# Kernel tuning notes

Hardware: AMD Instinct MI355X
Metric: run time of the kernel (lower is better)

The kernel has to match this reference:

```python
import jax, jax.numpy as jnp
import numpy as np

N, M, P, BATCH, T = 32, 8, 16, 64, 128
STD_DYN = 0.1
STD_OBS = 0.1


def _mT(x):
    return jnp.swapaxes(x, -1, -2)


def _sym(x):
    return 0.5 * (x + _mT(x))


def setup_inputs() -> dict:
    key = jax.random.key(0)
    ks = jax.random.split(key, 5)
    Y = jax.random.normal(ks[0], (BATCH, T, P), jnp.float32)
    U = jax.random.normal(ks[1], (BATCH, T, M), jnp.float32)
    # scale A so spectral radius < 1 -> stable covariance recursion over T steps
    A = jax.random.normal(ks[2], (BATCH, T, N, N), jnp.float32) * (0.5 / np.sqrt(N))
    B_mat = jax.random.normal(ks[3], (BATCH, T, N, M), jnp.float32) * 0.1
    C = jax.random.normal(ks[4], (BATCH, T, P, N), jnp.float32) * (1.0 / np.sqrt(N))
    mu0 = jnp.zeros((N,), jnp.float32)
    Sigma0 = jnp.eye(N, dtype=jnp.float32)  # SPD initial covariance
    return {"Y": Y, "U": U, "A": A, "B_mat": B_mat, "C": C, "mu0": mu0, "Sigma0": Sigma0}


def _kalman_smooth(Y, U, A, B_mat, C, mu0, Sigma0):
    b, t = Y.shape[0], Y.shape[1]
    n = mu0.shape[0]
    p = Y.shape[-1]
    dt = Y.dtype
    Q = (STD_DYN ** 2) * jnp.eye(n, dtype=dt)
    R = (STD_OBS ** 2) * jnp.eye(p, dtype=dt)
    I = jnp.eye(n, dtype=dt)
    tm = lambda x: jnp.moveaxis(x, 0, 1)  # [B,T,...] -> [T,B,...]

    # ---- forward filter (lax.scan over time, batched over B) ----
    def fstep(carry, x):
        mu, Sig = carry  # [b,n], [b,n,n]
        y, u, At, Bt, Ct = x
        mu_p = jnp.einsum('bij,bj->bi', At, mu) + jnp.einsum('bij,bj->bi', Bt, u)
        Sig_p = At @ Sig @ _mT(At) + Q
        r = y - jnp.einsum('bij,bj->bi', Ct, mu_p)
        S = _sym(Ct @ Sig_p @ _mT(Ct) + R)  # [b,p,p]
        # K = Sig_p C^T S^{-1}  (matches torch: solve(S, PCT.mT).mT)
        K = _mT(jnp.linalg.solve(S, _mT(Sig_p @ _mT(Ct))))  # [b,n,p]
        mu_f = mu_p + jnp.einsum('bij,bj->bi', K, r)
        IKC = I - K @ Ct
        Sig_f = _sym(IKC @ Sig_p @ _mT(IKC) + K @ R @ _mT(K))
        return (mu_f, Sig_f), (mu_f, Sig_f, mu_p, Sig_p)

    init = (jnp.broadcast_to(mu0, (b, n)), jnp.broadcast_to(Sigma0, (b, n, n)))
    A_tm = tm(A)
    _, (mu_f, Sig_f, mu_p, Sig_p) = jax.lax.scan(
        fstep, init, (tm(Y), tm(U), A_tm, tm(B_mat), tm(C)))

    # ---- RTS smoother (reverse scan) ----
    def sstep(carry, x):
        mu_s, Sig_s = carry
        Sf, Sp1, mf, mp1, At = x
        # J = Sig_f A^T Sig_pred^{-1} (matches torch: solve(Sp1.mT, (Sf@A.mT).mT).mT)
        J = _mT(jnp.linalg.solve(_mT(Sp1), _mT(Sf @ _mT(At))))
        mu_n = mf + jnp.einsum('bij,bj->bi', J, mu_s - mp1)
        Sig_n = _sym(Sf + J @ (Sig_s - Sp1) @ _mT(J))
        return (mu_n, Sig_n), (mu_n, Sig_n)

    xs = (Sig_f[:-1], Sig_p[1:], mu_f[:-1], mu_p[1:], A_tm[:-1])
    _, (mu_sm, Sig_sm) = jax.lax.scan(
        sstep, (mu_f[-1], Sig_f[-1]), xs, reverse=True)
    mu_sm = jnp.concatenate([mu_sm, mu_f[-1:]], axis=0)   # [T,b,n]
    Sig_sm = jnp.concatenate([Sig_sm, Sig_f[-1:]], axis=0)  # [T,b,n,n]
    mu_sm = jnp.moveaxis(mu_sm, 0, 1)
    Sig_sm = jnp.moveaxis(Sig_sm, 0, 1)
    # pack smoothed means + covariances into one array: [B,T,n,1+n]
    return jnp.concatenate([mu_sm[..., None], Sig_sm], axis=-1)


def reference(Y, U, A, B_mat, C, mu0, Sigma0):
    return _kalman_smooth(Y, U, A, B_mat, C, mu0, Sigma0)
```

## Files before the change

### kernel.cpp

```cpp
#include <hip/hip_runtime.h>

#define TT 128
#define NB 64
#define NSZ 32
#define MSZ 8
#define PSZ 16

typedef __attribute__((ext_vector_type(8)))  short bf16x8;
typedef __attribute__((ext_vector_type(16))) float f32x16;
typedef __attribute__((ext_vector_type(4)))  float f32x4;
typedef __attribute__((ext_vector_type(4)))  unsigned int uint4v;
typedef __attribute__((ext_vector_type(2)))  unsigned int uint2v;

union U8 { uint4v u; bf16x8 b; };

__device__ __forceinline__ float frcp(float x){ return __builtin_amdgcn_rcpf(x); }
__device__ __forceinline__ float rdl(float x, int lane){
  return __int_as_float(__builtin_amdgcn_readlane(__float_as_int(x), lane));
}

__device__ __forceinline__ unsigned int hipack(float x0, float x1){
  return __builtin_amdgcn_perm(__float_as_uint(x1), __float_as_uint(x0), 0x07060302u);
}
__device__ __forceinline__ unsigned int lopack(float x0, float x1){
  float l0 = x0 - __uint_as_float(__float_as_uint(x0) & 0xFFFF0000u);
  float l1 = x1 - __uint_as_float(__float_as_uint(x1) & 0xFFFF0000u);
  return __builtin_amdgcn_perm(__float_as_uint(l1), __float_as_uint(l0), 0x07060302u);
}
__device__ __forceinline__ unsigned int packhl(float x){
  unsigned int u = __float_as_uint(x);
  unsigned int h = u & 0xFFFF0000u;
  float xl = x - __uint_as_float(h);
  return h | (__float_as_uint(xl) >> 16);
}
__device__ __forceinline__ float unpk(unsigned int u){
  return __uint_as_float(u & 0xFFFF0000u) + __uint_as_float(u << 16);
}
__device__ __forceinline__ uint4v frag_hi(uint4v a, uint4v b){
  uint4v r;
  r.x = __builtin_amdgcn_perm(a.y, a.x, 0x07060302u);
  r.y = __builtin_amdgcn_perm(a.w, a.z, 0x07060302u);
  r.z = __builtin_amdgcn_perm(b.y, b.x, 0x07060302u);
  r.w = __builtin_amdgcn_perm(b.w, b.z, 0x07060302u);
  return r;
}
__device__ __forceinline__ uint4v frag_lo(uint4v a, uint4v b){
  uint4v r;
  r.x = __builtin_amdgcn_perm(a.y, a.x, 0x05040100u);
  r.y = __builtin_amdgcn_perm(a.w, a.z, 0x05040100u);
  r.z = __builtin_amdgcn_perm(b.y, b.x, 0x05040100u);
  r.w = __builtin_amdgcn_perm(b.w, b.z, 0x05040100u);
  return r;
}
__device__ __forceinline__ float blof(unsigned int h, unsigned int l){
  return __uint_as_float(h << 16) + __uint_as_float(l << 16);
}
__device__ __forceinline__ float bhif(unsigned int h, unsigned int l){
  return __uint_as_float(h & 0xFFFF0000u) + __uint_as_float(l & 0xFFFF0000u);
}
__device__ __forceinline__ f32x16 mfma32(bf16x8 a, bf16x8 b, f32x16 c){
  return __builtin_amdgcn_mfma_f32_32x32x16_bf16(a, b, c, 0, 0, 0);
}
__device__ __forceinline__ f32x4 mfma16(bf16x8 a, bf16x8 b, f32x4 c){
  return __builtin_amdgcn_mfma_f32_16x16x32_bf16(a, b, c, 0, 0, 0);
}
__device__ __forceinline__ void split16(float4 v0, float4 v1, float4 v2, float4 v3,
                                        unsigned short* hi, unsigned short* lo){
  uint4v hw0, hw1, lw0, lw1;
  hw0.x=hipack(v0.x,v0.y); hw0.y=hipack(v0.z,v0.w); hw0.z=hipack(v1.x,v1.y); hw0.w=hipack(v1.z,v1.w);
  hw1.x=hipack(v2.x,v2.y); hw1.y=hipack(v2.z,v2.w); hw1.z=hipack(v3.x,v3.y); hw1.w=hipack(v3.z,v3.w);
  lw0.x=lopack(v0.x,v0.y); lw0.y=lopack(v0.z,v0.w); lw0.z=lopack(v1.x,v1.y); lw0.w=lopack(v1.z,v1.w);
  lw1.x=lopack(v2.x,v2.y); lw1.y=lopack(v2.z,v2.w); lw1.z=lopack(v3.x,v3.y); lw1.w=lopack(v3.z,v3.w);
  *(uint4v*)hi = hw0; *(uint4v*)(hi+8) = hw1;
  *(uint4v*)lo = lw0; *(uint4v*)(lo+8) = lw1;
}
__device__ __forceinline__ void split8(float4 v0, float4 v1,
                                       unsigned short* hi, unsigned short* lo){
  uint4v hw, lw;
  hw.x=hipack(v0.x,v0.y); hw.y=hipack(v0.z,v0.w); hw.z=hipack(v1.x,v1.y); hw.w=hipack(v1.z,v1.w);
  lw.x=lopack(v0.x,v0.y); lw.y=lopack(v0.z,v0.w); lw.z=lopack(v1.x,v1.y); lw.w=lopack(v1.z,v1.w);
  *(uint4v*)hi = hw; *(uint4v*)lo = lw;
}
#define MK8(v0, v1, HI, LO) do { \
  (HI).u.x = hipack((v0).x,(v0).y); (HI).u.y = hipack((v0).z,(v0).w); \
  (HI).u.z = hipack((v1).x,(v1).y); (HI).u.w = hipack((v1).z,(v1).w); \
  (LO).u.x = lopack((v0).x,(v0).y); (LO).u.y = lopack((v0).z,(v0).w); \
  (LO).u.z = lopack((v1).x,(v1).y); (LO).u.w = lopack((v1).z,(v1).w); \
} while(0)

#define DLAYOUT_TO_BFRAG(uu, h, B_H0, B_L0, B_H1, B_L1) do { \
  float sw_[16]; \
  _Pragma("unroll") \
  for (int r_=0;r_<16;++r_) sw_[r_] = __shfl_xor((uu)[r_], 32); \
  float v0_[8], v1_[8]; \
  v0_[0]=(h)? sw_[4] :(uu)[0];  v0_[1]=(h)? sw_[5] :(uu)[1]; \
  v0_[2]=(h)? sw_[6] :(uu)[2];  v0_[3]=(h)? sw_[7] :(uu)[3]; \
  v0_[4]=(h)? (uu)[4]:sw_[0];   v0_[5]=(h)? (uu)[5]:sw_[1]; \
  v0_[6]=(h)? (uu)[6]:sw_[2];   v0_[7]=(h)? (uu)[7]:sw_[3]; \
  v1_[0]=(h)? sw_[12]:(uu)[8];  v1_[1]=(h)? sw_[13]:(uu)[9]; \
  v1_[2]=(h)? sw_[14]:(uu)[10]; v1_[3]=(h)? sw_[15]:(uu)[11]; \
  v1_[4]=(h)? (uu)[12]:sw_[8];  v1_[5]=(h)? (uu)[13]:sw_[9]; \
  v1_[6]=(h)? (uu)[14]:sw_[10]; v1_[7]=(h)? (uu)[15]:sw_[11]; \
  (B_H0).u.x=hipack(v0_[0],v0_[1]); (B_H0).u.y=hipack(v0_[2],v0_[3]); \
  (B_H0).u.z=hipack(v0_[4],v0_[5]); (B_H0).u.w=hipack(v0_[6],v0_[7]); \
  (B_L0).u.x=lopack(v0_[0],v0_[1]); (B_L0).u.y=lopack(v0_[2],v0_[3]); \
  (B_L0).u.z=lopack(v0_[4],v0_[5]); (B_L0).u.w=lopack(v0_[6],v0_[7]); \
  (B_H1).u.x=hipack(v1_[0],v1_[1]); (B_H1).u.y=hipack(v1_[2],v1_[3]); \
  (B_H1).u.z=hipack(v1_[4],v1_[5]); (B_H1).u.w=hipack(v1_[6],v1_[7]); \
  (B_L1).u.x=lopack(v1_[0],v1_[1]); (B_L1).u.y=lopack(v1_[2],v1_[3]); \
  (B_L1).u.z=lopack(v1_[4],v1_[5]); (B_L1).u.w=lopack(v1_[6],v1_[7]); \
} while(0)

__global__ __launch_bounds__(64) void kf_forward(
    const float* __restrict__ Yg, const float* __restrict__ Ug,
    const float* __restrict__ Ag, const float* __restrict__ Bg,
    const float* __restrict__ Cg, const float* __restrict__ mu0g,
    const float* __restrict__ Sig0g,
    float* __restrict__ outg, float* __restrict__ wsSig, float* __restrict__ wsMu)
{
  const int l   = threadIdx.x;
  const int b   = blockIdx.x;
  const int c32 = l & 31;
  const int h   = l >> 5;
  const int c16 = l & 15;
  const int q4  = l >> 4;
  const int kofA = h * 8;
  const int kofC = q4 * 8;
  const int rA = l >> 1, cA = (l & 1) << 4;
  const int rC = l >> 2, cC = (l & 3) << 3;

  __shared__ __align__(16) unsigned short Ahi[32][40], Alo[32][40];
  __shared__ __align__(16) unsigned short Chi[16][40], Clo[16][40];
  __shared__ __align__(16) unsigned short Ghi[32][40], Glo[32][40];
  __shared__ __align__(16) unsigned short Phi[32][40], Plo[32][40];
  __shared__ __align__(16) unsigned short Yhi[32][24], Ylo[32][24];
  __shared__ __align__(16) unsigned int   ZP[16][40];
  __shared__ __align__(16) unsigned int   KtTP[32][26];
  __shared__ __align__(16) float SLf[16][20];
  __shared__ __align__(16) float CSf[16][40];
  __shared__ __align__(16) float Bm[32][12];
  __shared__ __align__(16) float muf[32], mupf[32], rvf[16], yvf[16], uvf[8];

  const size_t bt0 = (size_t)b * TT;

  {
    const float* ap = Ag + bt0*1024 + rA*32 + cA;
    split16(*(const float4*)(ap+0), *(const float4*)(ap+4),
            *(const float4*)(ap+8), *(const float4*)(ap+12),
            &Ahi[rA][cA], &Alo[rA][cA]);
    const float* sp0 = Sig0g + rA*32 + cA;
    split16(*(const float4*)(sp0+0), *(const float4*)(sp0+4),
            *(const float4*)(sp0+8), *(const float4*)(sp0+12),
            &Ghi[rA][cA], &Glo[rA][cA]);
    const float* cp = Cg + bt0*512 + rC*32 + cC;
    split8(*(const float4*)(cp+0), *(const float4*)(cp+4),
           &Chi[rC][cC], &Clo[rC][cC]);
    *(float4*)&Bm[l>>1][(l&1)*4] = *(const float4*)(Bg + bt0*256 + (l>>1)*8 + (l&1)*4);
    if (l < 32) muf[l] = mu0g[l];
    if (l < 16) yvf[l] = Yg[bt0*16 + l];
    if (l < 8)  uvf[l] = Ug[bt0*8 + l];
  }

  for (int t = 0; t < TT; ++t) {
    const size_t bt = bt0 + t;

    U8 a_h0, a_h1, a_l0, a_l1, s_h0, s_h1, s_l0, s_l1;
    a_h0.u = *(const uint4v*)&Ahi[c32][0  + kofA];
    a_h1.u = *(const uint4v*)&Ahi[c32][16 + kofA];
    a_l0.u = *(const uint4v*)&Alo[c32][0  + kofA];
    a_l1.u = *(const uint4v*)&Alo[c32][16 + kofA];
    s_h0.u = *(const uint4v*)&Ghi[c32][0  + kofA];
    s_h1.u = *(const uint4v*)&Ghi[c32][16 + kofA];
    s_l0.u = *(const uint4v*)&Glo[c32][0  + kofA];
    s_l1.u = *(const uint4v*)&Glo[c32][16 + kofA];
    f32x16 t1a, t1b;
    #pragma unroll
    for (int r=0;r<16;++r){ t1a[r] = 0.f; t1b[r] = 0.f; }
    t1a = mfma32(s_h0.b, a_h0.b, t1a);
    t1a = mfma32(s_h0.b, a_l0.b, t1a);
    t1a = mfma32(s_l0.b, a_h0.b, t1a);
    t1b = mfma32(s_h1.b, a_h1.b, t1b);
    t1b = mfma32(s_h1.b, a_l1.b, t1b);
    t1b = mfma32(s_l1.b, a_h1.b, t1b);
    float uu[16];
    #pragma unroll
    for (int r=0;r<16;++r) uu[r] = t1a[r] + t1b[r];
    float part = 0.f;
    {
      float4 m0 = *(const float4*)&muf[kofA];
      float4 m1 = *(const float4*)&muf[kofA+4];
      float4 m2 = *(const float4*)&muf[16+kofA];
      float4 m3 = *(const float4*)&muf[16+kofA+4];
      part = fmaf(blof(a_h0.u.x,a_l0.u.x), m0.x, part);
      part = fmaf(bhif(a_h0.u.x,a_l0.u.x), m0.y, part);
      part = fmaf(blof(a_h0.u.y,a_l0.u.y), m0.z, part);
      part = fmaf(bhif(a_h0.u.y,a_l0.u.y), m0.w, part);
      part = fmaf(blof(a_h0.u.z,a_l0.u.z), m1.x, part);
      part = fmaf(bhif(a_h0.u.z,a_l0.u.z), m1.y, part);
      part = fmaf(blof(a_h0.u.w,a_l0.u.w), m1.z, part);
      part = fmaf(bhif(a_h0.u.w,a_l0.u.w), m1.w, part);
      part = fmaf(blof(a_h1.u.x,a_l1.u.x), m2.x, part);
      part = fmaf(bhif(a_h1.u.x,a_l1.u.x), m2.y, part);
      part = fmaf(blof(a_h1.u.y,a_l1.u.y), m2.z, part);
      part = fmaf(bhif(a_h1.u.y,a_l1.u.y), m2.w, part);
      part = fmaf(blof(a_h1.u.z,a_l1.u.z), m3.x, part);
      part = fmaf(bhif(a_h1.u.z,a_l1.u.z), m3.y, part);
      part = fmaf(blof(a_h1.u.w,a_l1.u.w), m3.z, part);
      part = fmaf(bhif(a_h1.u.w,a_l1.u.w), m3.w, part);
    }
    part += __shfl_xor(part, 32);
    {
      float4 b0 = *(const float4*)&Bm[c32][0];
      float4 b1 = *(const float4*)&Bm[c32][4];
      float4 u0 = *(const float4*)&uvf[0];
      float4 u1 = *(const float4*)&uvf[4];
      part = fmaf(b0.x,u0.x, fmaf(b0.y,u0.y, fmaf(b0.z,u0.z, fmaf(b0.w,u0.w, part))));
      part = fmaf(b1.x,u1.x, fmaf(b1.y,u1.y, fmaf(b1.z,u1.z, fmaf(b1.w,u1.w, part))));
    }
    if (l < 32){ mupf[c32] = part; wsMu[bt*32 + c32] = part; }

    U8 b_h0, b_h1, b_l0, b_l1;
    DLAYOUT_TO_BFRAG(uu, h, b_h0, b_l0, b_h1, b_l1);
    f32x16 spa, spb;
    #pragma unroll
    for (int r=0;r<16;++r){ spa[r] = 0.f; spb[r] = 0.f; }
    spa = mfma32(a_h0.b, b_h0.b, spa);
    spa = mfma32(a_h0.b, b_l0.b, spa);
    spa = mfma32(a_l0.b, b_h0.b, spa);
    spb = mfma32(a_h1.b, b_h1.b, spb);
    spb = mfma32(a_h1.b, b_l1.b, spb);
    spb = mfma32(a_l1.b, b_h1.b, spb);
    f32x16 sp;
    #pragma unroll
    for (int r=0;r<16;++r){
      int rr = (r&3) + 8*(r>>2) + 4*h;
      sp[r] = spa[r] + spb[r] + ((rr == c32) ? 0.01f : 0.f);
    }
    {
      float* wp = wsSig + (bt*32 + c32)*32;
      *(float4*)(wp + 0  + 4*h) = make_float4(sp[0], sp[1], sp[2], sp[3]);
      *(float4*)(wp + 8  + 4*h) = make_float4(sp[4], sp[5], sp[6], sp[7]);
      *(float4*)(wp + 16 + 4*h) = make_float4(sp[8], sp[9], sp[10],sp[11]);
      *(float4*)(wp + 24 + 4*h) = make_float4(sp[12],sp[13],sp[14],sp[15]);
      #pragma unroll
      for (int gq=0; gq<4; ++gq){
        uint2v hw, lw;
        hw.x = hipack(sp[4*gq+0], sp[4*gq+1]); hw.y = hipack(sp[4*gq+2], sp[4*gq+3]);
        lw.x = lopack(sp[4*gq+0], sp[4*gq+1]); lw.y = lopack(sp[4*gq+2], sp[4*gq+3]);
        *(uint2v*)&Phi[c32][8*gq + 4*h] = hw;
        *(uint2v*)&Plo[c32][8*gq + 4*h] = lw;
      }
    }

    U8 c_h, c_l, p_h0, p_l0, p_h1, p_l1;
    c_h.u  = *(const uint4v*)&Chi[c16][kofC];
    c_l.u  = *(const uint4v*)&Clo[c16][kofC];
    p_h0.u = *(const uint4v*)&Phi[c16][kofC];
    p_l0.u = *(const uint4v*)&Plo[c16][kofC];
    p_h1.u = *(const uint4v*)&Phi[16+c16][kofC];
    p_l1.u = *(const uint4v*)&Plo[16+c16][kofC];
    f32x4 cs0, cs1;
    #pragma unroll
    for (int r=0;r<4;++r){ cs0[r]=0.f; cs1[r]=0.f; }
    cs0 = mfma16(c_h.b, p_h0.b, cs0);
    cs0 = mfma16(c_h.b, p_l0.b, cs0);
    cs0 = mfma16(c_l.b, p_h0.b, cs0);
    cs1 = mfma16(c_h.b, p_h1.b, cs1);
    cs1 = mfma16(c_h.b, p_l1.b, cs1);
    cs1 = mfma16(c_l.b, p_h1.b, cs1);
    #pragma unroll
    for (int r=0;r<4;++r){
      int rr = q4*4 + r;
      ZP[rr][c16]     = packhl(cs0[r]);
      ZP[rr][16+c16]  = packhl(cs1[r]);
      CSf[rr][c16]    = cs0[r];
      CSf[rr][16+c16] = cs1[r];
    }
    {
      uint2v hw0, lw0, hw1, lw1;
      hw0.x = hipack(cs0[0],cs0[1]); hw0.y = hipack(cs0[2],cs0[3]);
      lw0.x = lopack(cs0[0],cs0[1]); lw0.y = lopack(cs0[2],cs0[3]);
      hw1.x = hipack(cs1[0],cs1[1]); hw1.y = hipack(cs1[2],cs1[3]);
      lw1.x = lopack(cs1[0],cs1[1]); lw1.y = lopack(cs1[2],cs1[3]);
      *(uint2v*)&Yhi[c16][q4*4]    = hw0; *(uint2v*)&Ylo[c16][q4*4]    = lw0;
      *(uint2v*)&Yhi[16+c16][q4*4] = hw1; *(uint2v*)&Ylo[16+c16][q4*4] = lw1;
    }
    {
      float prr = 0.f;
      float4 m0 = *(const float4*)&mupf[kofC];
      float4 m1 = *(const float4*)&mupf[kofC+4];
      prr = fmaf(blof(c_h.u.x,c_l.u.x), m0.x, prr);
      prr = fmaf(bhif(c_h.u.x,c_l.u.x), m0.y, prr);
      prr = fmaf(blof(c_h.u.y,c_l.u.y), m0.z, prr);
      prr = fmaf(bhif(c_h.u.y,c_l.u.y), m0.w, prr);
      prr = fmaf(blof(c_h.u.z,c_l.u.z), m1.x, prr);
      prr = fmaf(bhif(c_h.u.z,c_l.u.z), m1.y, prr);
      prr = fmaf(blof(c_h.u.w,c_l.u.w), m1.z, prr);
      prr = fmaf(bhif(c_h.u.w,c_l.u.w), m1.w, prr);
      prr += __shfl_xor(prr, 16);
      prr += __shfl_xor(prr, 32);
      if (l < 16) rvf[l] = yvf[l] - prr;
    }

    {
      U8 z_h, z_l;
      uint4v pz0 = *(const uint4v*)&ZP[c16][kofC];
      uint4v pz1 = *(const uint4v*)&ZP[c16][kofC+4];
      z_h.u = frag_hi(pz0, pz1); z_l.u = frag_lo(pz0, pz1);
      f32x4 ss;
      #pragma unroll
      for (int r=0;r<4;++r) ss[r] = 0.f;
      ss = mfma16(z_h.b, c_h.b, ss);
      ss = mfma16(z_h.b, c_l.b, ss);
      ss = mfma16(z_l.b, c_h.b, ss);
      #pragma unroll
      for (int r=0;r<4;++r){
        int rr = q4*4 + r;
        SLf[rr][c16] = ss[r] + ((rr == c16) ? 0.01f : 0.f);
      }
    }

    float4 pa0, pa1, pa2, pa3, pc0, pc1, pbv;
    float py = 0.f, pu = 0.f;
    pa0=pa1=pa2=pa3=make_float4(0.f,0.f,0.f,0.f);
    pc0=pc1=pbv=make_float4(0.f,0.f,0.f,0.f);
    if (t + 1 < TT){
      const float* ap = Ag + (bt+1)*1024 + rA*32 + cA;
      pa0 = *(const float4*)(ap+0);  pa1 = *(const float4*)(ap+4);
      pa2 = *(const float4*)(ap+8);  pa3 = *(const float4*)(ap+12);
      const float* cp = Cg + (bt+1)*512 + rC*32 + cC;
      pc0 = *(const float4*)(cp+0);  pc1 = *(const float4*)(cp+4);
      pbv = *(const float4*)(Bg + (bt+1)*256 + (l>>1)*8 + (l&1)*4);
      if (l < 16) py = Yg[(bt+1)*16 + l];
      if (l < 8)  pu = Ug[(bt+1)*8 + l];
    }

    {
      float aug[16];
      if (l < 16){
        #pragma unroll
        for (int i=0;i<16;++i) aug[i] = 0.5f*(SLf[i][l] + SLf[l][i]);
      } else if (l < 48){
        #pragma unroll
        for (int i=0;i<16;++i) aug[i] = CSf[i][l-16];
      } else {
        #pragma unroll
        for (int i=0;i<16;++i) aug[i] = 0.f;
      }
      #pragma unroll
      for (int k=0;k<16;++k){
        float piv = rdl(aug[k], k);
        float q = -aug[k] * frcp(piv);
        #pragma unroll
        for (int i=0;i<16;++i){
          if (i == k) continue;
          float s = rdl(aug[i], k);
          aug[i] = fmaf(q, s, aug[i]);
        }
      }
      if (l >= 16 && l < 48){
        #pragma unroll
        for (int i=0;i<16;++i){
          float d = rdl(aug[i], i);
          KtTP[l-16][i] = packhl(-aug[i] * frcp(d));
        }
      }
    }

    f32x16 sf = sp;
    {
      U8 y_h, y_l, kt_h, kt_l;
      y_h.u = *(const uint4v*)&Yhi[c32][8*h];
      y_l.u = *(const uint4v*)&Ylo[c32][8*h];
      uint4v k0, k1;
      { uint2v a0 = *(const uint2v*)&KtTP[c32][8*h];
        uint2v a1 = *(const uint2v*)&KtTP[c32][8*h+2];
        uint2v a2 = *(const uint2v*)&KtTP[c32][8*h+4];
        uint2v a3 = *(const uint2v*)&KtTP[c32][8*h+6];
        k0.x=a0.x; k0.y=a0.y; k0.z=a1.x; k0.w=a1.y;
        k1.x=a2.x; k1.y=a2.y; k1.z=a3.x; k1.w=a3.y; }
      kt_h.u = frag_hi(k0, k1); kt_l.u = frag_lo(k0, k1);
      sf = mfma32(y_h.b, kt_h.b, sf);
      sf = mfma32(y_h.b, kt_l.b, sf);
      sf = mfma32(y_l.b, kt_h.b, sf);
    }
    #pragma unroll
    for (int gq=0; gq<4; ++gq){
      uint2v hw, lw;
      hw.x = hipack(sf[4*gq+0], sf[4*gq+1]); hw.y = hipack(sf[4*gq+2], sf[4*gq+3]);
      lw.x = lopack(sf[4*gq+0], sf[4*gq+1]); lw.y = lopack(sf[4*gq+2], sf[4*gq+3]);
      *(uint2v*)&Ghi[c32][8*gq + 4*h] = hw;
      *(uint2v*)&Glo[c32][8*gq + 4*h] = lw;
    }
    {
      float* ob = outg + (bt*32)*33;
      #pragma unroll
      for (int r=0;r<16;++r){
        int rr = (r&3) + 8*(r>>2) + 4*h;
        ob[rr*33 + 1 + c32] = sf[r];
      }
      float mf = mupf[c32];
      #pragma unroll
      for (int p=0;p<16;++p){
        unsigned int w = KtTP[c32][p];
        mf = fmaf(-unpk(w), rvf[p], mf);
      }
      if (l < 32){ muf[c32] = mf; ob[c32*33] = mf; }
    }

    if (t + 1 < TT){
      split16(pa0, pa1, pa2, pa3, &Ahi[rA][cA], &Alo[rA][cA]);
      split8(pc0, pc1, &Chi[rC][cC], &Clo[rC][cC]);
      *(float4*)&Bm[l>>1][(l&1)*4] = pbv;
      if (l < 16) yvf[l] = py;
      if (l < 8)  uvf[l] = pu;
    }
  }
}

__global__ __launch_bounds__(64) void kf_precomp(
    const float* __restrict__ Ag, float* __restrict__ outg,
    float* __restrict__ wsSig, const float* __restrict__ wsMu)
{
  const int t = blockIdx.x;
  const int b = blockIdx.y;
  const int l = threadIdx.x;
  const int c32 = l & 31;
  const int h = l >> 5;
  const int kofA = h * 8;

  __shared__ __align__(16) float        Sffr[1060];
  __shared__ __align__(16) unsigned int MmP[32][34];
  __shared__ __align__(16) unsigned int VPT[32][34];
  __shared__ __align__(16) unsigned int JP [32][34];
  __shared__ float mp1f[32];

  const size_t bt = (size_t)b*TT + t;
  float* osl = outg + bt*1056;

  {
    const float4* src = (const float4*)osl;
    #pragma unroll
    for (int q=0;q<4;++q) *(float4*)&Sffr[(l + 64*q)*4] = src[l + 64*q];
    if (l < 8) *(float4*)&Sffr[(l + 256)*4] = src[l + 256];
    if (l < 32) mp1f[l] = wsMu[(bt+1)*32 + l];
  }

  float aug[32];
  if (l < 32){
    const float* pp = wsSig + (bt+1)*1024 + (size_t)l*32;
    #pragma unroll
    for (int q=0;q<8;++q){
      float4 v = *(const float4*)(pp + 4*q);
      aug[4*q]=v.x; aug[4*q+1]=v.y; aug[4*q+2]=v.z; aug[4*q+3]=v.w;
    }
  } else {
    #pragma unroll
    for (int i=0;i<32;++i) aug[i] = (i == l-32) ? 1.f : 0.f;
  }

  U8 a_h0, a_l0, a_h1, a_l1;
  {
    const float* ap = Ag + bt*1024 + c32*32;
    float4 v0 = *(const float4*)(ap + kofA);
    float4 v1 = *(const float4*)(ap + kofA + 4);
    float4 v2 = *(const float4*)(ap + 16 + kofA);
    float4 v3 = *(const float4*)(ap + 16 + kofA + 4);
    MK8(v0, v1, a_h0, a_l0);
    MK8(v2, v3, a_h1, a_l1);
  }
  U8 s_h0, s_l0, s_h1, s_l1;
  {
    const float* rp = &Sffr[c32*33 + 1];
    float4 v0, v1, v2, v3;
    v0.x=rp[kofA+0]; v0.y=rp[kofA+1]; v0.z=rp[kofA+2]; v0.w=rp[kofA+3];
    v1.x=rp[kofA+4]; v1.y=rp[kofA+5]; v1.z=rp[kofA+6]; v1.w=rp[kofA+7];
    v2.x=rp[16+kofA+0]; v2.y=rp[16+kofA+1]; v2.z=rp[16+kofA+2]; v2.w=rp[16+kofA+3];
    v3.x=rp[16+kofA+4]; v3.y=rp[16+kofA+5]; v3.z=rp[16+kofA+6]; v3.w=rp[16+kofA+7];
    MK8(v0, v1, s_h0, s_l0);
    MK8(v2, v3, s_h1, s_l1);
  }

  f32x16 ma, mb;
  #pragma unroll
  for (int r=0;r<16;++r){ ma[r]=0.f; mb[r]=0.f; }
  ma = mfma32(s_h0.b, a_h0.b, ma);
  ma = mfma32(s_h0.b, a_l0.b, ma);
  ma = mfma32(s_l0.b, a_h0.b, ma);
  mb = mfma32(s_h1.b, a_h1.b, mb);
  mb = mfma32(s_h1.b, a_l1.b, mb);
  mb = mfma32(s_l1.b, a_h1.b, mb);
  #pragma unroll
  for (int r=0;r<16;++r){
    int rr = (r&3) + 8*(r>>2) + 4*h;
    MmP[rr][c32] = packhl(ma[r] + mb[r]);
  }

  #pragma unroll
  for (int k=0;k<32;++k){
    float piv = rdl(aug[k], k);
    float q = -aug[k] * frcp(piv);
    #pragma unroll
    for (int i=0;i<32;++i){
      if (i == k) continue;
      float s = rdl(aug[i], k);
      aug[i] = fmaf(q, s, aug[i]);
    }
  }
  if (l >= 32){
    #pragma unroll
    for (int i=0;i<32;++i){
      float d = rdl(aug[i], i);
      VPT[l-32][i] = packhl(aug[i] * frcp(d));
    }
  }

  U8 m_h0, m_l0, m_h1, m_l1;
  {
    uint4v ua, ub, uc, ud;
    ua.x=MmP[c32][kofA+0]; ua.y=MmP[c32][kofA+1]; ua.z=MmP[c32][kofA+2]; ua.w=MmP[c32][kofA+3];
    ub.x=MmP[c32][kofA+4]; ub.y=MmP[c32][kofA+5]; ub.z=MmP[c32][kofA+6]; ub.w=MmP[c32][kofA+7];
    uc.x=MmP[c32][16+kofA+0]; uc.y=MmP[c32][16+kofA+1]; uc.z=MmP[c32][16+kofA+2]; uc.w=MmP[c32][16+kofA+3];
    ud.x=MmP[c32][16+kofA+4]; ud.y=MmP[c32][16+kofA+5]; ud.z=MmP[c32][16+kofA+6]; ud.w=MmP[c32][16+kofA+7];
    m_h0.u = frag_hi(ua, ub); m_l0.u = frag_lo(ua, ub);
    m_h1.u = frag_hi(uc, ud); m_l1.u = frag_lo(uc, ud);
  }
  U8 v_h0, v_l0, v_h1, v_l1;
  {
    uint4v ua, ub, uc, ud;
    ua.x=VPT[c32][kofA+0]; ua.y=VPT[c32][kofA+1]; ua.z=VPT[c32][kofA+2]; ua.w=VPT[c32][kofA+3];
    ub.x=VPT[c32][kofA+4]; ub.y=VPT[c32][kofA+5]; ub.z=VPT[c32][kofA+6]; ub.w=VPT[c32][kofA+7];
    uc.x=VPT[c32][16+kofA+0]; uc.y=VPT[c32][16+kofA+1]; uc.z=VPT[c32][16+kofA+2]; uc.w=VPT[c32][16+kofA+3];
    ud.x=VPT[c32][16+kofA+4]; ud.y=VPT[c32][16+kofA+5]; ud.z=VPT[c32][16+kofA+6]; ud.w=VPT[c32][16+kofA+7];
    v_h0.u = frag_hi(ua, ub); v_l0.u = frag_lo(ua, ub);
    v_h1.u = frag_hi(uc, ud); v_l1.u = frag_lo(uc, ud);
  }
  f32x16 ja, jb;
  #pragma unroll
  for (int r=0;r<16;++r){ ja[r]=0.f; jb[r]=0.f; }
  ja = mfma32(m_h0.b, v_h0.b, ja);
  ja = mfma32(m_h0.b, v_l0.b, ja);
  ja = mfma32(m_l0.b, v_h0.b, ja);
  jb = mfma32(m_h1.b, v_h1.b, jb);
  jb = mfma32(m_h1.b, v_l1.b, jb);
  jb = mfma32(m_l1.b, v_h1.b, jb);
  {
    float* jws = wsSig + (bt+1)*1024;
    #pragma unroll
    for (int r=0;r<16;++r){
      int rr = (r&3) + 8*(r>>2) + 4*h;
      float jv = ja[r] + jb[r];
      jws[rr*32 + c32] = jv;
      JP[rr][c32] = packhl(-jv);
    }
  }

  U8 nj_h0, nj_l0, nj_h1, nj_l1;
  {
    uint4v ua, ub, uc, ud;
    ua.x=JP[c32][kofA+0]; ua.y=JP[c32][kofA+1]; ua.z=JP[c32][kofA+2]; ua.w=JP[c32][kofA+3];
    ub.x=JP[c32][kofA+4]; ub.y=JP[c32][kofA+5]; ub.z=JP[c32][kofA+6]; ub.w=JP[c32][kofA+7];
    uc.x=JP[c32][16+kofA+0]; uc.y=JP[c32][16+kofA+1]; uc.z=JP[c32][16+kofA+2]; uc.w=JP[c32][16+kofA+3];
    ud.x=JP[c32][16+kofA+4]; ud.y=JP[c32][16+kofA+5]; ud.z=JP[c32][16+kofA+6]; ud.w=JP[c32][16+kofA+7];
    nj_h0.u = frag_hi(ua, ub); nj_l0.u = frag_lo(ua, ub);
    nj_h1.u = frag_hi(uc, ud); nj_l1.u = frag_lo(uc, ud);
  }
  f32x16 ea, eb;
  #pragma unroll
  for (int r=0;r<16;++r){
    int rr = (r&3) + 8*(r>>2) + 4*h;
    ea[r] = Sffr[rr*33 + 1 + c32];
    eb[r] = 0.f;
  }
  ea = mfma32(m_h0.b, nj_h0.b, ea);
  ea = mfma32(m_h0.b, nj_l0.b, ea);
  ea = mfma32(m_l0.b, nj_h0.b, ea);
  eb = mfma32(m_h1.b, nj_h1.b, eb);
  eb = mfma32(m_h1.b, nj_l1.b, eb);
  eb = mfma32(m_l1.b, nj_h1.b, eb);
  #pragma unroll
  for (int r=0;r<16;++r){
    int rr = (r&3) + 8*(r>>2) + 4*h;
    osl[rr*33 + 1 + c32] = ea[r] + eb[r];
  }

  {
    float e2 = Sffr[c32*33];
    #pragma unroll
    for (int k=0;k<32;++k)
      e2 = fmaf(unpk(JP[c32][k]), mp1f[k], e2);
    if (l < 32) osl[c32*33] = e2;
  }
}

__global__ __launch_bounds__(64) void kf_backward(
    float* __restrict__ outg, const float* __restrict__ wsSig)
{
  const int l   = threadIdx.x;
  const int b   = blockIdx.x;
  const int c32 = l & 31;
  const int h   = l >> 5;
  const int kofA = h * 8;
  const int rA = l >> 1, cA = (l & 1) << 4;

  __shared__ __align__(16) unsigned short Jhi[32][40], Jlo[32][40];
  __shared__ __align__(16) unsigned int   SP[32][36];
  __shared__ float muv[32];

  const size_t base = (size_t)b * TT;

  float er[16]; float ev;
  {
    const float* os = outg + (base + TT - 1)*32*33;
    const float* rp = os + rA*33 + 1 + cA;
    float4 v0 = *(const float4*)(rp+0), v1 = *(const float4*)(rp+4),
           v2 = *(const float4*)(rp+8), v3 = *(const float4*)(rp+12);
    uint4v u0, u1;
    u0.x = packhl(v0.x); u0.y = packhl(v0.y); u0.z = packhl(v0.z); u0.w = packhl(v0.w);
    u1.x = packhl(v1.x); u1.y = packhl(v1.y); u1.z = packhl(v1.z); u1.w = packhl(v1.w);
    *(uint4v*)&SP[rA][cA+0] = u0; *(uint4v*)&SP[rA][cA+4] = u1;
    u0.x = packhl(v2.x); u0.y = packhl(v2.y); u0.z = packhl(v2.z); u0.w = packhl(v2.w);
    u1.x = packhl(v3.x); u1.y = packhl(v3.y); u1.z = packhl(v3.z); u1.w = packhl(v3.w);
    *(uint4v*)&SP[rA][cA+8] = u0; *(uint4v*)&SP[rA][cA+12] = u1;
    if (l < 32) muv[l] = os[l*33];
    const float* jp = wsSig + ((base + TT - 1)*32 + rA)*32 + cA;
    split16(*(const float4*)(jp+0), *(const float4*)(jp+4),
            *(const float4*)(jp+8), *(const float4*)(jp+12),
            &Jhi[rA][cA], &Jlo[rA][cA]);
    const float* oe = outg + (base + TT - 2)*32*33;
    #pragma unroll
    for (int r=0;r<16;++r){
      int rr = (r&3) + 8*(r>>2) + 4*h;
      er[r] = oe[rr*33 + 1 + c32];
    }
    ev = (l < 32) ? oe[l*33] : 0.f;
  }

  for (int t = TT - 2; t >= 0; --t) {
    float4 pj0, pj1, pj2, pj3; float ner[16]; float nev = 0.f;
    if (t > 0) {
      const float* jp = wsSig + ((base + t)*32 + rA)*32 + cA;
      pj0 = *(const float4*)(jp+0);  pj1 = *(const float4*)(jp+4);
      pj2 = *(const float4*)(jp+8);  pj3 = *(const float4*)(jp+12);
      const float* oe = outg + (base + t - 1)*32*33;
      #pragma unroll
      for (int r=0;r<16;++r){
        int rr = (r&3) + 8*(r>>2) + 4*h;
        ner[r] = oe[rr*33 + 1 + c32];
      }
      if (l < 32) nev = oe[l*33];
    } else {
      pj0=pj1=pj2=pj3=make_float4(0.f,0.f,0.f,0.f);
      #pragma unroll
      for (int r=0;r<16;++r) ner[r] = 0.f;
    }

    U8 a_h0, a_h1, a_l0, a_l1;
    a_h0.u = *(const uint4v*)&Jhi[c32][0  + kofA];
    a_h1.u = *(const uint4v*)&Jhi[c32][16 + kofA];
    a_l0.u = *(const uint4v*)&Jlo[c32][0  + kofA];
    a_l1.u = *(const uint4v*)&Jlo[c32][16 + kofA];
    U8 s_h0, s_l0, s_h1, s_l1;
    {
      uint4v ua = *(const uint4v*)&SP[c32][0  + kofA];
      uint4v ub = *(const uint4v*)&SP[c32][4  + kofA];
      uint4v uc = *(const uint4v*)&SP[c32][16 + kofA];
      uint4v ud = *(const uint4v*)&SP[c32][20 + kofA];
      s_h0.u = frag_hi(ua, ub); s_l0.u = frag_lo(ua, ub);
      s_h1.u = frag_hi(uc, ud); s_l1.u = frag_lo(uc, ud);
    }
    f32x16 wa, wb;
    #pragma unroll
    for (int r=0;r<16;++r){ wa[r]=0.f; wb[r]=0.f; }
    wa = mfma32(s_h0.b, a_h0.b, wa);
    wa = mfma32(s_h0.b, a_l0.b, wa);
    wa = mfma32(s_l0.b, a_h0.b, wa);
    wb = mfma32(s_h1.b, a_h1.b, wb);
    wb = mfma32(s_h1.b, a_l1.b, wb);
    wb = mfma32(s_l1.b, a_h1.b, wb);
    float ww[16];
    #pragma unroll
    for (int r=0;r<16;++r) ww[r] = wa[r] + wb[r];

    U8 bw_h0, bw_l0, bw_h1, bw_l1;
    DLAYOUT_TO_BFRAG(ww, h, bw_h0, bw_l0, bw_h1, bw_l1);
    f32x16 ga, gb;
    #pragma unroll
    for (int r=0;r<16;++r){ ga[r] = er[r]; gb[r] = 0.f; }
    ga = mfma32(a_h0.b, bw_h0.b, ga);
    ga = mfma32(a_h0.b, bw_l0.b, ga);
    ga = mfma32(a_l0.b, bw_h0.b, ga);
    gb = mfma32(a_h1.b, bw_h1.b, gb);
    gb = mfma32(a_h1.b, bw_l1.b, gb);
    gb = mfma32(a_l1.b, bw_h1.b, gb);

    float part = 0.f;
    {
      float4 m0 = *(const float4*)&muv[kofA];
      float4 m1 = *(const float4*)&muv[kofA+4];
      float4 m2 = *(const float4*)&muv[16+kofA];
      float4 m3 = *(const float4*)&muv[16+kofA+4];
      part = fmaf(blof(a_h0.u.x,a_l0.u.x), m0.x, part);
      part = fmaf(bhif(a_h0.u.x,a_l0.u.x), m0.y, part);
      part = fmaf(blof(a_h0.u.y,a_l0.u.y), m0.z, part);
      part = fmaf(bhif(a_h0.u.y,a_l0.u.y), m0.w, part);
      part = fmaf(blof(a_h0.u.z,a_l0.u.z), m1.x, part);
      part = fmaf(bhif(a_h0.u.z,a_l0.u.z), m1.y, part);
      part = fmaf(blof(a_h0.u.w,a_l0.u.w), m1.z, part);
      part = fmaf(bhif(a_h0.u.w,a_l0.u.w), m1.w, part);
      part = fmaf(blof(a_h1.u.x,a_l1.u.x), m2.x, part);
      part = fmaf(bhif(a_h1.u.x,a_l1.u.x), m2.y, part);
      part = fmaf(blof(a_h1.u.y,a_l1.u.y), m2.z, part);
      part = fmaf(bhif(a_h1.u.y,a_l1.u.y), m2.w, part);
      part = fmaf(blof(a_h1.u.z,a_l1.u.z), m3.x, part);
      part = fmaf(bhif(a_h1.u.z,a_l1.u.z), m3.y, part);
      part = fmaf(blof(a_h1.u.w,a_l1.u.w), m3.z, part);
      part = fmaf(bhif(a_h1.u.w,a_l1.u.w), m3.w, part);
    }
    part += __shfl_xor(part, 32);
    float mn = ev + part;

    {
      float* ob = outg + ((base + t)*32)*33;
      #pragma unroll
      for (int r=0;r<16;++r){
        int rr = (r&3) + 8*(r>>2) + 4*h;
        ob[rr*33 + 1 + c32] = ga[r] + gb[r];
      }
      #pragma unroll
      for (int gq=0; gq<4; ++gq){
        uint4v uw;
        uw.x = packhl(ga[4*gq+0]+gb[4*gq+0]); uw.y = packhl(ga[4*gq+1]+gb[4*gq+1]);
        uw.z = packhl(ga[4*gq+2]+gb[4*gq+2]); uw.w = packhl(ga[4*gq+3]+gb[4*gq+3]);
        *(uint4v*)&SP[c32][8*gq + 4*h] = uw;
      }
      if (l < 32){ muv[l] = mn; ob[l*33] = mn; }
    }

    if (t > 0){
      split16(pj0, pj1, pj2, pj3, &Jhi[rA][cA], &Jlo[rA][cA]);
      #pragma unroll
      for (int r=0;r<16;++r) er[r] = ner[r];
      ev = nev;
    }
  }
}

extern "C" void kernel_launch(void* const* d_in, const int* in_sizes, int n_in,
                              void* d_out, int out_size, void* d_ws, size_t ws_size,
                              hipStream_t stream) {
  (void)in_sizes; (void)n_in; (void)out_size; (void)ws_size;
  const float* Yg   = (const float*)d_in[0];
  const float* Ug   = (const float*)d_in[1];
  const float* Ag   = (const float*)d_in[2];
  const float* Bg   = (const float*)d_in[3];
  const float* Cg   = (const float*)d_in[4];
  const float* mu0g = (const float*)d_in[5];
  const float* S0g  = (const float*)d_in[6];
  float* outg = (float*)d_out;
  float* wsSig = (float*)d_ws;
  float* wsMu  = wsSig + (size_t)NB*TT*NSZ*NSZ;

  hipLaunchKernelGGL(kf_forward, dim3(NB), dim3(64), 0, stream,
                     Yg, Ug, Ag, Bg, Cg, mu0g, S0g, outg, wsSig, wsMu);
  hipLaunchKernelGGL(kf_precomp, dim3(TT-1, NB), dim3(64), 0, stream,
                     Ag, outg, wsSig, wsMu);
  hipLaunchKernelGGL(kf_backward, dim3(NB), dim3(64), 0, stream,
                     outg, wsSig);
}
```

Baseline: 704.0 us.

## Process two batches per wavefront in backward smoother and load J directly to registers

The backward RTS kernel now has each 64-thread block run two independent batch recursions interleaved, so the launch uses half as many blocks. Interleaving the two chains is meant to hide MFMA and memory latency along the serial time dependence. J fragments are loaded straight from global memory into registers and split into bf16 hi/lo parts in registers, which removes the Jhi/Jlo shared-memory staging. The cost is more register pressure and only 32 workgroups, which occupy fewer CUs. MK8 is assumed to be defined in the part of the file not shown.

```diff
diff --git a/kernel.cpp b/kernel.cpp
--- a/kernel.cpp
+++ b/kernel.cpp
@@ -597,151 +597,171 @@
     float* __restrict__ outg, const float* __restrict__ wsSig)
 {
   const int l   = threadIdx.x;
-  const int b   = blockIdx.x;
   const int c32 = l & 31;
   const int h   = l >> 5;
   const int kofA = h * 8;
   const int rA = l >> 1, cA = (l & 1) << 4;
 
-  __shared__ __align__(16) unsigned short Jhi[32][40], Jlo[32][40];
-  __shared__ __align__(16) unsigned int   SP[32][36];
-  __shared__ float muv[32];
-
-  const size_t base = (size_t)b * TT;
-
-  float er[16]; float ev;
-  {
-    const float* os = outg + (base + TT - 1)*32*33;
+  __shared__ __align__(16) unsigned int SP[2][32][36];
+  __shared__ float muv[2][32];
+
+  size_t base[2];
+  base[0] = (size_t)(blockIdx.x*2 + 0) * TT;
+  base[1] = (size_t)(blockIdx.x*2 + 1) * TT;
+
+  float er[2][16]; float ev[2];
+  float4 pj[2][4];
+
+  #pragma unroll
+  for (int bb=0;bb<2;++bb){
+    const float* os = outg + (base[bb] + TT - 1)*1056;
     const float* rp = os + rA*33 + 1 + cA;
     float4 v0 = *(const float4*)(rp+0), v1 = *(const float4*)(rp+4),
            v2 = *(const float4*)(rp+8), v3 = *(const float4*)(rp+12);
     uint4v u0, u1;
     u0.x = packhl(v0.x); u0.y = packhl(v0.y); u0.z = packhl(v0.z); u0.w = packhl(v0.w);
     u1.x = packhl(v1.x); u1.y = packhl(v1.y); u1.z = packhl(v1.z); u1.w = packhl(v1.w);
-    *(uint4v*)&SP[rA][cA+0] = u0; *(uint4v*)&SP[rA][cA+4] = u1;
+    *(uint4v*)&SP[bb][rA][cA+0] = u0; *(uint4v*)&SP[bb][rA][cA+4] = u1;
     u0.x = packhl(v2.x); u0.y = packhl(v2.y); u0.z = packhl(v2.z); u0.w = packhl(v2.w);
     u1.x = packhl(v3.x); u1.y = packhl(v3.y); u1.z = packhl(v3.z); u1.w = packhl(v3.w);
-    *(uint4v*)&SP[rA][cA+8] = u0; *(uint4v*)&SP[rA][cA+12] = u1;
-    if (l < 32) muv[l] = os[l*33];
-    const float* jp = wsSig + ((base + TT - 1)*32 + rA)*32 + cA;
-    split16(*(const float4*)(jp+0), *(const float4*)(jp+4),
-            *(const float4*)(jp+8), *(const float4*)(jp+12),
-            &Jhi[rA][cA], &Jlo[rA][cA]);
-    const float* oe = outg + (base + TT - 2)*32*33;
+    *(uint4v*)&SP[bb][rA][cA+8] = u0; *(uint4v*)&SP[bb][rA][cA+12] = u1;
+    if (l < 32) muv[bb][l] = os[l*33];
+    const float* jp = wsSig + (base[bb] + TT - 1)*1024 + c32*32;
+    pj[bb][0] = *(const float4*)(jp + kofA);
+    pj[bb][1] = *(const float4*)(jp + kofA + 4);
+    pj[bb][2] = *(const float4*)(jp + 16 + kofA);
+    pj[bb][3] = *(const float4*)(jp + 16 + kofA + 4);
+    const float* oe = outg + (base[bb] + TT - 2)*1056;
     #pragma unroll
     for (int r=0;r<16;++r){
       int rr = (r&3) + 8*(r>>2) + 4*h;
-      er[r] = oe[rr*33 + 1 + c32];
-    }
-    ev = (l < 32) ? oe[l*33] : 0.f;
+      er[bb][r] = oe[rr*33 + 1 + c32];
+    }
+    ev[bb] = (l < 32) ? oe[l*33] : 0.f;
   }
 
   for (int t = TT - 2; t >= 0; --t) {
-    float4 pj0, pj1, pj2, pj3; float ner[16]; float nev = 0.f;
+    float4 nj[2][4]; float ner[2][16]; float nev[2];
     if (t > 0) {
-      const float* jp = wsSig + ((base + t)*32 + rA)*32 + cA;
-      pj0 = *(const float4*)(jp+0);  pj1 = *(const float4*)(jp+4);
-      pj2 = *(const float4*)(jp+8);  pj3 = *(const float4*)(jp+12);
-      const float* oe = outg + (base + t - 1)*32*33;
-      #pragma unroll
-      for (int r=0;r<16;++r){
-        int rr = (r&3) + 8*(r>>2) + 4*h;
-        ner[r] = oe[rr*33 + 1 + c32];
-      }
-      if (l < 32) nev = oe[l*33];
+      #pragma unroll
+      for (int bb=0;bb<2;++bb){
+        const float* jp = wsSig + (base[bb] + t)*1024 + c32*32;
+        nj[bb][0] = *(const float4*)(jp + kofA);
+        nj[bb][1] = *(const float4*)(jp + kofA + 4);
+        nj[bb][2] = *(const float4*)(jp + 16 + kofA);
+        nj[bb][3] = *(const float4*)(jp + 16 + kofA + 4);
+        const float* oe = outg + (base[bb] + t - 1)*1056;
+        #pragma unroll
+        for (int r=0;r<16;++r){
+          int rr = (r&3) + 8*(r>>2) + 4*h;
+          ner[bb][r] = oe[rr*33 + 1 + c32];
+        }
+        nev[bb] = (l < 32) ? oe[l*33] : 0.f;
+      }
     } else {
-      pj0=pj1=pj2=pj3=make_float4(0.f,0.f,0.f,0.f);
-      #pragma unroll
-      for (int r=0;r<16;++r) ner[r] = 0.f;
-    }
-
-    U8 a_h0, a_h1, a_l0, a_l1;
-    a_h0.u = *(const uint4v*)&Jhi[c32][0  + kofA];
-    a_h1.u = *(const uint4v*)&Jhi[c32][16 + kofA];
-    a_l0.u = *(const uint4v*)&Jlo[c32][0  + kofA];
-    a_l1.u = *(const uint4v*)&Jlo[c32][16 + kofA];
-    U8 s_h0, s_l0, s_h1, s_l1;
-    {
-      uint4v ua = *(const uint4v*)&SP[c32][0  + kofA];
-      uint4v ub = *(const uint4v*)&SP[c32][4  + kofA];
-      uint4v uc = *(const uint4v*)&SP[c32][16 + kofA];
-      uint4v ud = *(const uint4v*)&SP[c32][20 + kofA];
+      #pragma unroll
+      for (int bb=0;bb<2;++bb){
+        nj[bb][0]=nj[bb][1]=nj[bb][2]=nj[bb][3]=make_float4(0.f,0.f,0.f,0.f);
+        #pragma unroll
+        for (int r=0;r<16;++r) ner[bb][r] = 0.f;
+        nev[bb] = 0.f;
+      }
+    }
+
+    U8 aH0[2], aL0[2], aH1[2], aL1[2];
+    #pragma unroll
+    for (int bb=0;bb<2;++bb){
+      MK8(pj[bb][0], pj[bb][1], aH0[bb], aL0[bb]);
+      MK8(pj[bb][2], pj[bb][3], aH1[bb], aL1[bb]);
+    }
+
+    float ww[2][16];
+    #pragma unroll
+    for (int bb=0;bb<2;++bb){
+      U8 s_h0, s_l0, s_h1, s_l1;
+      uint4v ua = *(const uint4v*)&SP[bb][c32][0  + kofA];
+      uint4v ub = *(const uint4v*)&SP[bb][c32][4  + kofA];
+      uint4v uc = *(const uint4v*)&SP[bb][c32][16 + kofA];
+      uint4v ud = *(const uint4v*)&SP[bb][c32][20 + kofA];
       s_h0.u = frag_hi(ua, ub); s_l0.u = frag_lo(ua, ub);
       s_h1.u = frag_hi(uc, ud); s_l1.u = frag_lo(uc, ud);
-    }
-    f32x16 wa, wb;
-    #pragma unroll
-    for (int r=0;r<16;++r){ wa[r]=0.f; wb[r]=0.f; }
-    wa = mfma32(s_h0.b, a_h0.b, wa);
-    wa = mfma32(s_h0.b, a_l0.b, wa);
-    wa = mfma32(s_l0.b, a_h0.b, wa);
-    wb = mfma32(s_h1.b, a_h1.b, wb);
-    wb = mfma32(s_h1.b, a_l1.b, wb);
-    wb = mfma32(s_l1.b, a_h1.b, wb);
-    float ww[16];
-    #pragma unroll
-    for (int r=0;r<16;++r) ww[r] = wa[r] + wb[r];
-
-    U8 bw_h0, bw_l0, bw_h1, bw_l1;
-    DLAYOUT_TO_BFRAG(ww, h, bw_h0, bw_l0, bw_h1, bw_l1);
-    f32x16 ga, gb;
-    #pragma unroll
-    for (int r=0;r<16;++r){ ga[r] = er[r]; gb[r] = 0.f; }
-    ga = mfma32(a_h0.b, bw_h0.b, ga);
-    ga = mfma32(a_h0.b, bw_l0.b, ga);
-    ga = mfma32(a_l0.b, bw_h0.b, ga);
-    gb = mfma32(a_h1.b, bw_h1.b, gb);
-    gb = mfma32(a_h1.b, bw_l1.b, gb);
-    gb = mfma32(a_l1.b, bw_h1.b, gb);
-
-    float part = 0.f;
-    {
-      float4 m0 = *(const float4*)&muv[kofA];
-      float4 m1 = *(const float4*)&muv[kofA+4];
-      float4 m2 = *(const float4*)&muv[16+kofA];
-      float4 m3 = *(const float4*)&muv[16+kofA+4];
-      part = fmaf(blof(a_h0.u.x,a_l0.u.x), m0.x, part);
-      part = fmaf(bhif(a_h0.u.x,a_l0.u.x), m0.y, part);
-      part = fmaf(blof(a_h0.u.y,a_l0.u.y), m0.z, part);
-      part = fmaf(bhif(a_h0.u.y,a_l0.u.y), m0.w, part);
-      part = fmaf(blof(a_h0.u.z,a_l0.u.z), m1.x, part);
-      part = fmaf(bhif(a_h0.u.z,a_l0.u.z), m1.y, part);
-      part = fmaf(blof(a_h0.u.w,a_l0.u.w), m1.z, part);
-      part = fmaf(bhif(a_h0.u.w,a_l0.u.w), m1.w, part);
-      part = fmaf(blof(a_h1.u.x,a_l1.u.x), m2.x, part);
-      part = fmaf(bhif(a_h1.u.x,a_l1.u.x), m2.y, part);
-      part = fmaf(blof(a_h1.u.y,a_l1.u.y), m2.z, part);
-      part = fmaf(bhif(a_h1.u.y,a_l1.u.y), m2.w, part);
-      part = fmaf(blof(a_h1.u.z,a_l1.u.z), m3.x, part);
-      part = fmaf(bhif(a_h1.u.z,a_l1.u.z), m3.y, part);
-      part = fmaf(blof(a_h1.u.w,a_l1.u.w), m3.z, part);
-      part = fmaf(bhif(a_h1.u.w,a_l1.u.w), m3.w, part);
-    }
-    part += __shfl_xor(part, 32);
-    float mn = ev + part;
-
-    {
-      float* ob = outg + ((base + t)*32)*33;
-      #pragma unroll
-      for (int r=0;r<16;++r){
-        int rr = (r&3) + 8*(r>>2) + 4*h;
-        ob[rr*33 + 1 + c32] = ga[r] + gb[r];
-      }
-      #pragma unroll
-      for (int gq=0; gq<4; ++gq){
-        uint4v uw;
-        uw.x = packhl(ga[4*gq+0]+gb[4*gq+0]); uw.y = packhl(ga[4*gq+1]+gb[4*gq+1]);
-        uw.z = packhl(ga[4*gq+2]+gb[4*gq+2]); uw.w = packhl(ga[4*gq+3]+gb[4*gq+3]);
-        *(uint4v*)&SP[c32][8*gq + 4*h] = uw;
-      }
-      if (l < 32){ muv[l] = mn; ob[l*33] = mn; }
-    }
-
-    if (t > 0){
-      split16(pj0, pj1, pj2, pj3, &Jhi[rA][cA], &Jlo[rA][cA]);
-      #pragma unroll
-      for (int r=0;r<16;++r) er[r] = ner[r];
-      ev = nev;
+      f32x16 wa, wb;
+      #pragma unroll
+      for (int r=0;r<16;++r){ wa[r]=0.f; wb[r]=0.f; }
+      wa = mfma32(s_h0.b, aH0[bb].b, wa);
+      wa = mfma32(s_h0.b, aL0[bb].b, wa);
+      wa = mfma32(s_l0.b, aH0[bb].b, wa);
+      wb = mfma32(s_h1.b, aH1[bb].b, wb);
+      wb = mfma32(s_h1.b, aL1[bb].b, wb);
+      wb = mfma32(s_l1.b, aH1[bb].b, wb);
+      #pragma unroll
+      for (int r=0;r<16;++r) ww[bb][r] = wa[r] + wb[r];
+    }
+
+    #pragma unroll
+    for (int bb=0;bb<2;++bb){
+      U8 bw_h0, bw_l0, bw_h1, bw_l1;
+      DLAYOUT_TO_BFRAG(ww[bb], h, bw_h0, bw_l0, bw_h1, bw_l1);
+      f32x16 ga, gb;
+      #pragma unroll
+      for (int r=0;r<16;++r){ ga[r] = er[bb][r]; gb[r] = 0.f; }
+      ga = mfma32(aH0[bb].b, bw_h0.b, ga);
+      ga = mfma32(aH0[bb].b, bw_l0.b, ga);
+      ga = mfma32(aL0[bb].b, bw_h0.b, ga);
+      gb = mfma32(aH1[bb].b, bw_h1.b, gb);
+      gb = mfma32(aH1[bb].b, bw_l1.b, gb);
+      gb = mfma32(aL1[bb].b, bw_h1.b, gb);
+
+      float part = 0.f;
+      {
+        float4 m0 = *(const float4*)&muv[bb][kofA];
+        float4 m1 = *(const float4*)&muv[bb][kofA+4];
+        float4 m2 = *(const float4*)&muv[bb][16+kofA];
+        float4 m3 = *(const float4*)&muv[bb][16+kofA+4];
+        part = fmaf(blof(aH0[bb].u.x,aL0[bb].u.x), m0.x, part);
+        part = fmaf(bhif(aH0[bb].u.x,aL0[bb].u.x), m0.y, part);
+        part = fmaf(blof(aH0[bb].u.y,aL0[bb].u.y), m0.z, part);
+        part = fmaf(bhif(aH0[bb].u.y,aL0[bb].u.y), m0.w, part);
+        part = fmaf(blof(aH0[bb].u.z,aL0[bb].u.z), m1.x, part);
+        part = fmaf(bhif(aH0[bb].u.z,aL0[bb].u.z), m1.y, part);
+        part = fmaf(blof(aH0[bb].u.w,aL0[bb].u.w), m1.z, part);
+        part = fmaf(bhif(aH0[bb].u.w,aL0[bb].u.w), m1.w, part);
+        part = fmaf(blof(aH1[bb].u.x,aL1[bb].u.x), m2.x, part);
+        part = fmaf(bhif(aH1[bb].u.x,aL1[bb].u.x), m2.y, part);
+        part = fmaf(blof(aH1[bb].u.y,aL1[bb].u.y), m2.z, part);
+        part = fmaf(bhif(aH1[bb].u.y,aL1[bb].u.y), m2.w, part);
+        part = fmaf(blof(aH1[bb].u.z,aL1[bb].u.z), m3.x, part);
+        part = fmaf(bhif(aH1[bb].u.z,aL1[bb].u.z), m3.y, part);
+        part = fmaf(blof(aH1[bb].u.w,aL1[bb].u.w), m3.z, part);
+        part = fmaf(bhif(aH1[bb].u.w,aL1[bb].u.w), m3.w, part);
+      }
+      part += __shfl_xor(part, 32);
+      float mn = ev[bb] + part;
+
+      {
+        float* ob = outg + (base[bb] + t)*1056;
+        #pragma unroll
+        for (int r=0;r<16;++r){
+          int rr = (r&3) + 8*(r>>2) + 4*h;
+          ob[rr*33 + 1 + c32] = ga[r] + gb[r];
+        }
+        #pragma unroll
+        for (int gq=0; gq<4; ++gq){
+          uint4v uw;
+          uw.x = packhl(ga[4*gq+0]+gb[4*gq+0]); uw.y = packhl(ga[4*gq+1]+gb[4*gq+1]);
+          uw.z = packhl(ga[4*gq+2]+gb[4*gq+2]); uw.w = packhl(ga[4*gq+3]+gb[4*gq+3]);
+          *(uint4v*)&SP[bb][c32][8*gq + 4*h] = uw;
+        }
+        if (l < 32){ muv[bb][l] = mn; ob[l*33] = mn; }
+      }
+
+      if (t > 0){
+        #pragma unroll
+        for (int q=0;q<4;++q) pj[bb][q] = nj[bb][q];
+        #pragma unroll
+        for (int r=0;r<16;++r) er[bb][r] = ner[bb][r];
+        ev[bb] = nev[bb];
+      }
     }
   }
 }
@@ -765,6 +785,6 @@
                      Yg, Ug, Ag, Bg, Cg, mu0g, S0g, outg, wsSig, wsMu);
   hipLaunchKernelGGL(kf_precomp, dim3(TT-1, NB), dim3(64), 0, stream,
                      Ag, outg, wsSig, wsMu);
-  hipLaunchKernelGGL(kf_backward, dim3(NB), dim3(64), 0, stream,
+  hipLaunchKernelGGL(kf_backward, dim3(NB/2), dim3(64), 0, stream,
                      outg, wsSig);
 }
```

New measurement: 841.9 us. 1.2x slower.
